# Optimization experiments

Hardware: AMD Instinct MI355X
Metric: run time of the kernel (lower is better)

## Reference

```python
import jax, jax.numpy as jnp
import numpy as np

N = 50000   # nodes
E = 800000  # edges (before self-loops)
D = 128     # feature dim
B = 1024    # query batch
EPS = 1e-5


def setup_inputs() -> dict:
    key = jax.random.key(0)
    ks = jax.random.split(key, 24)
    rn = lambda k, s, sc=0.05: jax.random.normal(k, s, jnp.float32) * sc
    return {
        "x": jax.random.randint(ks[0], (B, 3), 0, N),
        "edge_index": jax.random.randint(ks[1], (2, E), 0, N),
        "emb": rn(ks[2], (N, D), 1.0),
        # GAT layer 1
        "W1": rn(ks[3], (D, D)), "att_src1": rn(ks[4], (D,)), "att_dst1": rn(ks[5], (D,)), "b1": jnp.zeros((D,), jnp.float32),
        "gn1_w": jnp.ones((D,), jnp.float32), "gn1_b": jnp.zeros((D,), jnp.float32), "gn1_ms": jnp.ones((D,), jnp.float32),
        # GAT layer 2
        "W2": rn(ks[6], (D, D)), "att_src2": rn(ks[7], (D,)), "att_dst2": rn(ks[8], (D,)), "b2": jnp.zeros((D,), jnp.float32),
        "gn2_w": jnp.ones((D,), jnp.float32), "gn2_b": jnp.zeros((D,), jnp.float32), "gn2_ms": jnp.ones((D,), jnp.float32),
        # head
        "lin1_W": rn(ks[9], (3 * D, 3 * D)), "lin1_b": jnp.zeros((3 * D,), jnp.float32),
        "bn_w": jnp.ones((3 * D,), jnp.float32), "bn_b": jnp.zeros((3 * D,), jnp.float32),
        "lin2_W": rn(ks[10], (N, 3 * D)), "lin2_b": jnp.zeros((N,), jnp.float32),
    }


def _gat(h_in, src, dst, W, a_src, a_dst, b, n):
    # PyG GATConv, heads=1, negative_slope=0.2, self-loops already in src/dst,
    # dropout inactive (eval). Messages flow src -> dst.
    h = h_in @ W.T                                   # [N, D]
    as_n = h @ a_src                                 # [N]
    ad_n = h @ a_dst                                 # [N]
    e = jax.nn.leaky_relu(as_n[src] + ad_n[dst], 0.2)  # [E']
    m = jax.ops.segment_max(e, dst, num_segments=n)
    ex = jnp.exp(e - m[dst])
    den = jax.ops.segment_sum(ex, dst, num_segments=n)
    alpha = ex / den[dst]                            # segment softmax over dst
    out = jax.ops.segment_sum(h[src] * alpha[:, None], dst, num_segments=n)
    return out + b


def _graph_norm(h, w, b, ms):
    # PyG GraphNorm, single graph: per-feature mean/var over all nodes
    mu = h.mean(axis=0)
    out = h - mu * ms
    var = (out * out).mean(axis=0)
    return out / jnp.sqrt(var + EPS) * w + b


def reference(x, edge_index, emb, W1, att_src1, att_dst1, b1, gn1_w, gn1_b, gn1_ms,
              W2, att_src2, att_dst2, b2, gn2_w, gn2_b, gn2_ms,
              lin1_W, lin1_b, bn_w, bn_b, lin2_W, lin2_b):
    loop = jnp.arange(N)
    src = jnp.concatenate([edge_index[0], loop])
    dst = jnp.concatenate([edge_index[1], loop])

    h = jax.nn.relu(_graph_norm(_gat(emb, src, dst, W1, att_src1, att_dst1, b1, N), gn1_w, gn1_b, gn1_ms))
    h = jax.nn.relu(_graph_norm(_gat(h, src, dst, W2, att_src2, att_dst2, b2, N), gn2_w, gn2_b, gn2_ms))

    z = jnp.concatenate([h[x[:, 0]], h[x[:, 1]], h[x[:, 2]]], axis=1)  # [B, 3D]
    z = z @ lin1_W.T + lin1_b
    mu = z.mean(axis=0)
    var = ((z - mu) ** 2).mean(axis=0)  # BatchNorm1d training-mode batch stats
    z = jax.nn.relu((z - mu) / jnp.sqrt(var + EPS) * bn_w + bn_b)
    z = z @ lin2_W.T + lin2_b
    return jax.nn.log_softmax(z, axis=-1)
```

## Files before the change

### kernel.cpp

```cpp
#include <hip/hip_runtime.h>
#include <cstdint>
#include <cstddef>

#define NN 50000
#define EE 800000
#define EP 850000
#define DD 128
#define BB 1024
#define D3 384
#define NEG_SLOPE 0.2f

typedef __attribute__((ext_vector_type(8))) short short8;
typedef __attribute__((ext_vector_type(4))) float f32x4;

__device__ __forceinline__ unsigned short f2bf(float f) {
  unsigned int u = __float_as_uint(f);
  u += 0x7fffu + ((u >> 16) & 1u);
  return (unsigned short)(u >> 16);
}

__global__ void k_count(const int* __restrict__ eidx, int* __restrict__ cnt) {
  int e = blockIdx.x * 256 + threadIdx.x;
  if (e >= EP) return;
  int d = (e < EE) ? eidx[EE + e] : (e - EE);
  atomicAdd(&cnt[d], 1);
}

__global__ void k_scan1(const int* __restrict__ cnt, int* __restrict__ offs, int* __restrict__ bsum) {
  __shared__ int sd[1024];
  int tid = threadIdx.x;
  int i = blockIdx.x * 1024 + tid;
  int v = (i < NN) ? cnt[i] : 0;
  sd[tid] = v;
  __syncthreads();
  for (int off = 1; off < 1024; off <<= 1) {
    int t = (tid >= off) ? sd[tid - off] : 0;
    __syncthreads();
    sd[tid] += t;
    __syncthreads();
  }
  if (i < NN) offs[i] = sd[tid] - v;
  if (tid == 1023) bsum[blockIdx.x] = sd[1023];
}

__global__ void k_scan2(const int* __restrict__ bsum, int* __restrict__ bso) {
  int lane = threadIdx.x;
  int v = (lane < 49) ? bsum[lane] : 0;
  int s = v;
  #pragma unroll
  for (int off = 1; off < 64; off <<= 1) {
    int t = __shfl_up(s, off, 64);
    if (lane >= off) s += t;
  }
  if (lane < 49) bso[lane] = s - v;
}

__global__ void k_scan3(int* __restrict__ offs, const int* __restrict__ bso, int* __restrict__ cur) {
  int i = blockIdx.x * 256 + threadIdx.x;
  if (i >= NN) return;
  int o = offs[i] + bso[i >> 10];
  offs[i] = o;
  cur[i] = o;
}

__global__ void k_scatter(const int* __restrict__ eidx, int* __restrict__ cur, int* __restrict__ ssrc) {
  int e = blockIdx.x * 256 + threadIdx.x;
  if (e >= EP) return;
  int s, d;
  if (e < EE) { s = eidx[e]; d = eidx[EE + e]; } else { s = e - EE; d = s; }
  int p = atomicAdd(&cur[d], 1);
  ssrc[p] = s;
}

template<bool ABF16>
__global__ __launch_bounds__(256) void gemm_mfma(const void* __restrict__ Ap_, const float* __restrict__ Bm,
                                                 const float* __restrict__ bias, float* __restrict__ C,
                                                 int M, int Ncols, int K) {
  int tid = threadIdx.x;
  int wv = tid >> 6, lane = tid & 63;
  int l15 = lane & 15, q = lane >> 4;
  int n0 = blockIdx.x * 64;
  int mbase = blockIdx.y * 256 + wv * 64;
  int arow[4], brow[4];
  float bs[4];
  #pragma unroll
  for (int mi = 0; mi < 4; mi++) {
    int r = mbase + mi * 16 + l15;
    arow[mi] = (r < M) ? r : (M - 1);
  }
  #pragma unroll
  for (int nt = 0; nt < 4; nt++) {
    int col = n0 + nt * 16 + l15;
    brow[nt] = (col < Ncols) ? col : (Ncols - 1);
    bs[nt] = (bias != nullptr && col < Ncols) ? bias[col] : 0.0f;
  }
  f32x4 acc[4][4] = {};
  int nks = K >> 5;
  for (int ks = 0; ks < nks; ks++) {
    int k0 = ks * 32 + q * 8;
    short8 a[4], b[4];
    #pragma unroll
    for (int mi = 0; mi < 4; mi++) {
      if constexpr (ABF16) {
        a[mi] = *(const short8*)((const unsigned short*)Ap_ + (size_t)arow[mi] * K + k0);
      } else {
        const float* p = (const float*)Ap_ + (size_t)arow[mi] * K + k0;
        float4 v0 = *(const float4*)p, v1 = *(const float4*)(p + 4);
        short8 t;
        t[0] = f2bf(v0.x); t[1] = f2bf(v0.y); t[2] = f2bf(v0.z); t[3] = f2bf(v0.w);
        t[4] = f2bf(v1.x); t[5] = f2bf(v1.y); t[6] = f2bf(v1.z); t[7] = f2bf(v1.w);
        a[mi] = t;
      }
    }
    #pragma unroll
    for (int nt = 0; nt < 4; nt++) {
      const float* p = Bm + (size_t)brow[nt] * K + k0;
      float4 v0 = *(const float4*)p, v1 = *(const float4*)(p + 4);
      short8 t;
      t[0] = f2bf(v0.x); t[1] = f2bf(v0.y); t[2] = f2bf(v0.z); t[3] = f2bf(v0.w);
      t[4] = f2bf(v1.x); t[5] = f2bf(v1.y); t[6] = f2bf(v1.z); t[7] = f2bf(v1.w);
      b[nt] = t;
    }
    #pragma unroll
    for (int mi = 0; mi < 4; mi++)
      #pragma unroll
      for (int nt = 0; nt < 4; nt++)
        acc[mi][nt] = __builtin_amdgcn_mfma_f32_16x16x32_bf16(a[mi], b[nt], acc[mi][nt], 0, 0, 0);
  }
  #pragma unroll
  for (int mi = 0; mi < 4; mi++) {
    #pragma unroll
    for (int nt = 0; nt < 4; nt++) {
      int col = n0 + nt * 16 + l15;
      if (col < Ncols) {
        int rowb = mbase + mi * 16 + q * 4;
        #pragma unroll
        for (int r = 0; r < 4; r++) {
          int row = rowb + r;
          if (row < M) C[(size_t)row * Ncols + col] = acc[mi][nt][r] + bs[nt];
        }
      }
    }
  }
}

__global__ __launch_bounds__(256) void gemm_abt(const float* __restrict__ A, const float* __restrict__ Bm,
                                                const float* __restrict__ bias, float* __restrict__ C,
                                                int M, int Ncols, int K) {
  __shared__ float As[32][66];
  __shared__ float Bs[32][66];
  int tid = threadIdx.x;
  int tx = tid & 15, ty = tid >> 4;
  int m0 = blockIdx.x * 64, n0 = blockIdx.y * 64;
  float acc[4][4] = {};
  int lr = tid >> 2, lc = (tid & 3) * 8;
  for (int k0 = 0; k0 < K; k0 += 32) {
    float4 av0 = make_float4(0.f,0.f,0.f,0.f), av1 = av0, bv0 = av0, bv1 = av0;
    if (m0 + lr < M) {
      const float* Ap = A + (size_t)(m0 + lr) * K + k0 + lc;
      av0 = *(const float4*)Ap; av1 = *(const float4*)(Ap + 4);
    }
    if (n0 + lr < Ncols) {
      const float* Bp = Bm + (size_t)(n0 + lr) * K + k0 + lc;
      bv0 = *(const float4*)Bp; bv1 = *(const float4*)(Bp + 4);
    }
    __syncthreads();
    As[lc + 0][lr] = av0.x; As[lc + 1][lr] = av0.y; As[lc + 2][lr] = av0.z; As[lc + 3][lr] = av0.w;
    As[lc + 4][lr] = av1.x; As[lc + 5][lr] = av1.y; As[lc + 6][lr] = av1.z; As[lc + 7][lr] = av1.w;
    Bs[lc + 0][lr] = bv0.x; Bs[lc + 1][lr] = bv0.y; Bs[lc + 2][lr] = bv0.z; Bs[lc + 3][lr] = bv0.w;
    Bs[lc + 4][lr] = bv1.x; Bs[lc + 5][lr] = bv1.y; Bs[lc + 6][lr] = bv1.z; Bs[lc + 7][lr] = bv1.w;
    __syncthreads();
    #pragma unroll
    for (int kk = 0; kk < 32; kk++) {
      float a[4], b[4];
      #pragma unroll
      for (int i = 0; i < 4; i++) a[i] = As[kk][ty * 4 + i];
      #pragma unroll
      for (int j = 0; j < 4; j++) b[j] = Bs[kk][tx * 4 + j];
      #pragma unroll
      for (int i = 0; i < 4; i++)
        #pragma unroll
        for (int j = 0; j < 4; j++)
          acc[i][j] += a[i] * b[j];
    }
  }
  #pragma unroll
  for (int i = 0; i < 4; i++) {
    int row = m0 + ty * 4 + i;
    if (row < M) {
      #pragma unroll
      for (int j = 0; j < 4; j++) {
        int col = n0 + tx * 4 + j;
        if (col < Ncols) {
          float v = acc[i][j];
          if (bias) v += bias[col];
          C[(size_t)row * Ncols + col] = v;
        }
      }
    }
  }
}

__global__ void k_attn(const float* __restrict__ h, const float* __restrict__ asrc, const float* __restrict__ adst,
                       float* __restrict__ as_, float* __restrict__ ad_) {
  int wid = (blockIdx.x * 256 + threadIdx.x) >> 6;
  int lane = threadIdx.x & 63;
  if (wid >= NN) return;
  float v0 = h[(size_t)wid * DD + lane];
  float v1 = h[(size_t)wid * DD + 64 + lane];
  float s = v0 * asrc[lane] + v1 * asrc[64 + lane];
  float d = v0 * adst[lane] + v1 * adst[64 + lane];
  #pragma unroll
  for (int o = 32; o; o >>= 1) { s += __shfl_xor(s, o, 64); d += __shfl_xor(d, o, 64); }
  if (lane == 0) { as_[wid] = s; ad_[wid] = d; }
}

__global__ void k_agg(const float* __restrict__ h, const float* __restrict__ as_, const float* __restrict__ ad_,
                      const int* __restrict__ offs, const int* __restrict__ cnt, const int* __restrict__ ssrc,
                      const float* __restrict__ bias, float* __restrict__ outp) {
  int wid = (blockIdx.x * 256 + threadIdx.x) >> 6;
  int lane = threadIdx.x & 63;
  if (wid >= NN) return;
  int start = offs[wid], deg = cnt[wid];
  float add = ad_[wid];
  float m = -3.0e38f;
  for (int i = lane; i < deg; i += 64) {
    int s = ssrc[start + i];
    float e = as_[s] + add;
    e = (e >= 0.0f) ? e : NEG_SLOPE * e;
    m = fmaxf(m, e);
  }
  #pragma unroll
  for (int o = 32; o; o >>= 1) m = fmaxf(m, __shfl_xor(m, o, 64));
  float den = 0.0f;
  for (int i = lane; i < deg; i += 64) {
    int s = ssrc[start + i];
    float e = as_[s] + add;
    e = (e >= 0.0f) ? e : NEG_SLOPE * e;
    den += __expf(e - m);
  }
  #pragma unroll
  for (int o = 32; o; o >>= 1) den += __shfl_xor(den, o, 64);
  float a0 = 0.0f, a1 = 0.0f;
  for (int i = 0; i < deg; i++) {
    int s = ssrc[start + i];
    float e = as_[s] + add;
    e = (e >= 0.0f) ? e : NEG_SLOPE * e;
    float wg = __expf(e - m);
    a0 += wg * h[(size_t)s * DD + lane];
    a1 += wg * h[(size_t)s * DD + 64 + lane];
  }
  float inv = 1.0f / den;
  outp[(size_t)wid * DD + lane]      = a0 * inv + bias[lane];
  outp[(size_t)wid * DD + 64 + lane] = a1 * inv + bias[64 + lane];
}

__global__ void k_gn_stats(const float* __restrict__ h, float* __restrict__ acc) {
  __shared__ float r1[256], r2[256];
  int tid = threadIdx.x;
  int f = tid & 127, rg = tid >> 7;
  float a = 0.0f, b = 0.0f;
  for (int r = blockIdx.x * 2 + rg; r < NN; r += gridDim.x * 2) {
    float v = h[(size_t)r * DD + f];
    a += v; b += v * v;
  }
  r1[tid] = a; r2[tid] = b;
  __syncthreads();
  if (tid < 128) {
    atomicAdd(&acc[f], r1[tid] + r1[tid + 128]);
    atomicAdd(&acc[DD + f], r2[tid] + r2[tid + 128]);
  }
}

__global__ void k_gn_apply(float* __restrict__ h, const float* __restrict__ acc,
                           const float* __restrict__ ms, const float* __restrict__ w, const float* __restrict__ b) {
  const float invN = 1.0f / NN;
  for (size_t i = (size_t)blockIdx.x * 256 + threadIdx.x; i < (size_t)NN * DD; i += (size_t)gridDim.x * 256) {
    int f = (int)(i & 127);
    float mu = acc[f] * invN;
    float qm = acc[DD + f] * invN;
    float sub = mu * ms[f];
    float var = qm - 2.0f * sub * mu + sub * sub;
    float v = (h[i] - sub) * rsqrtf(var + 1e-5f) * w[f] + b[f];
    h[i] = fmaxf(v, 0.0f);
  }
}

__global__ void k_gather(const float* __restrict__ h, const int* __restrict__ x, float* __restrict__ z1) {
  int i = blockIdx.x * 256 + threadIdx.x;
  if (i >= BB * D3) return;
  int b = i / D3, t = i - b * D3;
  int part = t >> 7, f = t & 127;
  int node = x[b * 3 + part];
  z1[i] = h[(size_t)node * DD + f];
}

__global__ void k_bn(const float* __restrict__ z, const float* __restrict__ w, const float* __restrict__ b,
                     unsigned short* __restrict__ zb) {
  int c = blockIdx.x;
  int lane = threadIdx.x;
  float s = 0.0f, s2 = 0.0f;
  for (int r = lane; r < BB; r += 64) {
    float v = z[(size_t)r * D3 + c];
    s += v; s2 += v * v;
  }
  #pragma unroll
  for (int o = 32; o; o >>= 1) { s += __shfl_xor(s, o, 64); s2 += __shfl_xor(s2, o, 64); }
  float mu = s * (1.0f / BB);
  float var = s2 * (1.0f / BB) - mu * mu;
  float sc = rsqrtf(var + 1e-5f) * w[c];
  float sb = b[c];
  for (int r = lane; r < BB; r += 64) {
    float v = (z[(size_t)r * D3 + c] - mu) * sc + sb;
    zb[(size_t)r * D3 + c] = f2bf(fmaxf(v, 0.0f));
  }
}

__global__ __launch_bounds__(256) void k_softmax(float* __restrict__ z) {
  __shared__ float sm[256], ss[256];
  int row = blockIdx.x, tid = threadIdx.x;
  float* zr = z + (size_t)row * NN;
  float m = -3.0e38f, s = 0.0f;
  for (int c = tid; c < NN; c += 256) {
    float v = zr[c];
    if (v > m) { s *= __expf(m - v); m = v; }
    s += __expf(v - m);
  }
  sm[tid] = m; ss[tid] = s;
  __syncthreads();
  for (int st = 128; st > 0; st >>= 1) {
    if (tid < st) {
      float m2 = sm[tid + st], s2 = ss[tid + st];
      float M = fmaxf(sm[tid], m2);
      ss[tid] = ss[tid] * __expf(sm[tid] - M) + s2 * __expf(m2 - M);
      sm[tid] = M;
    }
    __syncthreads();
  }
  float L = sm[0] + logf(ss[0]);
  for (int c = tid; c < NN; c += 256) zr[c] -= L;
}

extern "C" void kernel_launch(void* const* d_in, const int* in_sizes, int n_in,
                              void* d_out, int out_size, void* d_ws, size_t ws_size,
                              hipStream_t stream) {
  const int*   x     = (const int*)d_in[0];
  const int*   eidx  = (const int*)d_in[1];
  const float* emb   = (const float*)d_in[2];
  const float* W1    = (const float*)d_in[3];
  const float* as1   = (const float*)d_in[4];
  const float* ad1   = (const float*)d_in[5];
  const float* b1    = (const float*)d_in[6];
  const float* gn1w  = (const float*)d_in[7];
  const float* gn1b  = (const float*)d_in[8];
  const float* gn1ms = (const float*)d_in[9];
  const float* W2    = (const float*)d_in[10];
  const float* as2   = (const float*)d_in[11];
  const float* ad2   = (const float*)d_in[12];
  const float* b2    = (const float*)d_in[13];
  const float* gn2w  = (const float*)d_in[14];
  const float* gn2b  = (const float*)d_in[15];
  const float* gn2ms = (const float*)d_in[16];
  const float* l1W   = (const float*)d_in[17];
  const float* l1b   = (const float*)d_in[18];
  const float* bnw   = (const float*)d_in[19];
  const float* bnb   = (const float*)d_in[20];
  const float* l2W   = (const float*)d_in[21];
  const float* l2b   = (const float*)d_in[22];
  float* out = (float*)d_out;

  float* h1 = out;
  float* h2 = out + (size_t)NN * DD;

  char* wsb = (char*)d_ws;
  size_t o = 0;
  auto alloc = [&](size_t bytes) -> void* {
    void* p = wsb + o;
    o = (o + bytes + 255) & ~(size_t)255;
    return p;
  };
  int*   ssrc = (int*)alloc((size_t)EP * 4);
  int*   cnt  = (int*)alloc((size_t)NN * 4);
  int*   offs = (int*)alloc((size_t)NN * 4);
  int*   cur  = (int*)alloc((size_t)NN * 4);
  float* as_  = (float*)alloc((size_t)NN * 4);
  float* ad_  = (float*)alloc((size_t)NN * 4);
  int*   bsum = (int*)alloc(64 * 4);
  int*   bso  = (int*)alloc(64 * 4);
  float* gnacc= (float*)alloc(2 * DD * 4);
  float* z1   = (float*)alloc((size_t)BB * D3 * 4);
  float* z2   = (float*)alloc((size_t)BB * D3 * 4);
  unsigned short* zbf = (unsigned short*)alloc((size_t)BB * D3 * 2);

  hipMemsetAsync(cnt, 0, (size_t)NN * 4, stream);
  k_count  <<<(EP + 255) / 256, 256, 0, stream>>>(eidx, cnt);
  k_scan1  <<<49, 1024, 0, stream>>>(cnt, offs, bsum);
  k_scan2  <<<1, 64, 0, stream>>>(bsum, bso);
  k_scan3  <<<(NN + 255) / 256, 256, 0, stream>>>(offs, bso, cur);
  k_scatter<<<(EP + 255) / 256, 256, 0, stream>>>(eidx, cur, ssrc);

  gemm_mfma<false><<<dim3(2, 196), 256, 0, stream>>>(emb, W1, nullptr, h1, NN, DD, DD);
  k_attn  <<<(NN + 3) / 4, 256, 0, stream>>>(h1, as1, ad1, as_, ad_);
  k_agg   <<<(NN + 3) / 4, 256, 0, stream>>>(h1, as_, ad_, offs, cnt, ssrc, b1, h2);
  hipMemsetAsync(gnacc, 0, 2 * DD * 4, stream);
  k_gn_stats<<<256, 256, 0, stream>>>(h2, gnacc);
  k_gn_apply<<<8192, 256, 0, stream>>>(h2, gnacc, gn1ms, gn1w, gn1b);

  gemm_mfma<false><<<dim3(2, 196), 256, 0, stream>>>(h2, W2, nullptr, h1, NN, DD, DD);
  k_attn  <<<(NN + 3) / 4, 256, 0, stream>>>(h1, as2, ad2, as_, ad_);
  k_agg   <<<(NN + 3) / 4, 256, 0, stream>>>(h1, as_, ad_, offs, cnt, ssrc, b2, h2);
  hipMemsetAsync(gnacc, 0, 2 * DD * 4, stream);
  k_gn_stats<<<256, 256, 0, stream>>>(h2, gnacc);
  k_gn_apply<<<8192, 256, 0, stream>>>(h2, gnacc, gn2ms, gn2w, gn2b);

  k_gather<<<(BB * D3 + 255) / 256, 256, 0, stream>>>(h2, x, z1);
  gemm_abt<<<dim3(16, 6), 256, 0, stream>>>(z1, l1W, l1b, z2, BB, D3, D3);
  k_bn    <<<D3, 64, 0, stream>>>(z2, bnw, bnb, zbf);
  gemm_mfma<true><<<dim3(782, 4), 256, 0, stream>>>(zbf, l2W, l2b, out, BB, NN, D3);
  k_softmax<<<BB, 256, 0, stream>>>(out);
}
```

Baseline: 1.203 ms.

## Switch GNN pipeline to bf16 intermediates with LDS-tiled MFMA GEMM

Replaces the register-direct MFMA GEMM and the scalar FP32 head GEMM with one LDS-tiled 128x128 bf16 MFMA kernel that uses global_load_lds and swizzled shared memory. Embeddings and weights are pre-converted to bf16, and the GAT projected features are stored in bf16, which halves the gather traffic in the attention and aggregation kernels. The aggregation loop is also unrolled by four to overlap gathers. The aim is to cut memory bandwidth in the edge aggregation and the large final GEMM, at the cost of lower precision for intermediate features and extra conversion passes.

```diff
diff --git a/kernel.cpp b/kernel.cpp
--- a/kernel.cpp
+++ b/kernel.cpp
@@ -12,11 +12,30 @@
 
 typedef __attribute__((ext_vector_type(8))) short short8;
 typedef __attribute__((ext_vector_type(4))) float f32x4;
-
-__device__ __forceinline__ unsigned short f2bf(float f) {
-  unsigned int u = __float_as_uint(f);
+typedef unsigned short u16;
+typedef unsigned int u32;
+
+__device__ __forceinline__ u16 f2bf(float f) {
+  u32 u = __float_as_uint(f);
   u += 0x7fffu + ((u >> 16) & 1u);
-  return (unsigned short)(u >> 16);
+  return (u16)(u >> 16);
+}
+__device__ __forceinline__ float bflo(u32 u) { return __uint_as_float(u << 16); }
+__device__ __forceinline__ float bfhi(u32 u) { return __uint_as_float(u & 0xffff0000u); }
+
+__device__ __forceinline__ void gl2lds16(const u16* g, u16* lds_base_uniform) {
+  __builtin_amdgcn_global_load_lds((const __attribute__((address_space(1))) u32*)g,
+                                   (__attribute__((address_space(3))) u32*)lds_base_uniform,
+                                   16, 0, 0);
+}
+
+__global__ void k_f2bf(const float* __restrict__ s, u16* __restrict__ d, int n4) {
+  int i = blockIdx.x * 256 + threadIdx.x;
+  if (i >= n4) return;
+  float4 v = ((const float4*)s)[i];
+  ushort4 o;
+  o.x = f2bf(v.x); o.y = f2bf(v.y); o.z = f2bf(v.z); o.w = f2bf(v.w);
+  ((ushort4*)d)[i] = o;
 }
 
 __global__ void k_count(const int* __restrict__ eidx, int* __restrict__ cnt) {
@@ -72,150 +91,126 @@
   ssrc[p] = s;
 }
 
-template<bool ABF16>
-__global__ __launch_bounds__(256) void gemm_mfma(const void* __restrict__ Ap_, const float* __restrict__ Bm,
-                                                 const float* __restrict__ bias, float* __restrict__ C,
-                                                 int M, int Ncols, int K) {
+template<bool B_IS_F32, bool OUT_BF16>
+__global__ __launch_bounds__(256) void gemm_tile(const u16* __restrict__ A, const void* __restrict__ Bv,
+                                                 const float* __restrict__ bias, void* __restrict__ Cv,
+                                                 int M, int N, int K) {
+  __shared__ u16 As[16 * 512];
+  __shared__ u16 Bs[16 * 512];
   int tid = threadIdx.x;
-  int wv = tid >> 6, lane = tid & 63;
+  int w = tid >> 6, lane = tid & 63;
   int l15 = lane & 15, q = lane >> 4;
-  int n0 = blockIdx.x * 64;
-  int mbase = blockIdx.y * 256 + wv * 64;
-  int arow[4], brow[4];
-  float bs[4];
-  #pragma unroll
-  for (int mi = 0; mi < 4; mi++) {
-    int r = mbase + mi * 16 + l15;
-    arow[mi] = (r < M) ? r : (M - 1);
-  }
-  #pragma unroll
-  for (int nt = 0; nt < 4; nt++) {
-    int col = n0 + nt * 16 + l15;
-    brow[nt] = (col < Ncols) ? col : (Ncols - 1);
-    bs[nt] = (bias != nullptr && col < Ncols) ? bias[col] : 0.0f;
-  }
+  int n0 = blockIdx.x * 128, m0 = blockIdx.y * 128;
+  int mh = w & 1, nh = w >> 1;
+
+  int lr = lane >> 3;
+  int cg = (lane & 7) ^ lr;
+
   f32x4 acc[4][4] = {};
-  int nks = K >> 5;
-  for (int ks = 0; ks < nks; ks++) {
-    int k0 = ks * 32 + q * 8;
-    short8 a[4], b[4];
+
+  for (int kt = 0; kt < K; kt += 64) {
     #pragma unroll
-    for (int mi = 0; mi < 4; mi++) {
-      if constexpr (ABF16) {
-        a[mi] = *(const short8*)((const unsigned short*)Ap_ + (size_t)arow[mi] * K + k0);
-      } else {
-        const float* p = (const float*)Ap_ + (size_t)arow[mi] * K + k0;
-        float4 v0 = *(const float4*)p, v1 = *(const float4*)(p + 4);
+    for (int i = 0; i < 4; i++) {
+      int inst = (w << 2) | i;
+      int row = inst * 8 + lr;
+      int grow = m0 + row; if (grow > M - 1) grow = M - 1;
+      gl2lds16(A + (size_t)grow * K + kt + cg * 8, &As[inst * 512]);
+    }
+    if constexpr (!B_IS_F32) {
+      const u16* Bb = (const u16*)Bv;
+      #pragma unroll
+      for (int i = 0; i < 4; i++) {
+        int inst = (w << 2) | i;
+        int row = inst * 8 + lr;
+        int gn = n0 + row; if (gn > N - 1) gn = N - 1;
+        gl2lds16(Bb + (size_t)gn * K + kt + cg * 8, &Bs[inst * 512]);
+      }
+    } else {
+      const float* Bf = (const float*)Bv;
+      int row = tid >> 1, half = tid & 1;
+      int gn = n0 + row; if (gn > N - 1) gn = N - 1;
+      const float* gp = Bf + (size_t)gn * K + kt;
+      #pragma unroll
+      for (int j = 0; j < 4; j++) {
+        int c = half * 4 + j;
+        float4 v0 = *(const float4*)(gp + c * 8);
+        float4 v1 = *(const float4*)(gp + c * 8 + 4);
         short8 t;
         t[0] = f2bf(v0.x); t[1] = f2bf(v0.y); t[2] = f2bf(v0.z); t[3] = f2bf(v0.w);
         t[4] = f2bf(v1.x); t[5] = f2bf(v1.y); t[6] = f2bf(v1.z); t[7] = f2bf(v1.w);
-        a[mi] = t;
+        int c2 = c ^ (row & 7);
+        *(short8*)(&Bs[row * 64 + c2 * 8]) = t;
       }
     }
+    __builtin_amdgcn_s_waitcnt(0x0f70);
+    __syncthreads();
+
+    #pragma unroll
+    for (int kk = 0; kk < 2; kk++) {
+      short8 a[4], b[4];
+      int cbase = kk * 4 + q;
+      int csw = cbase ^ (l15 & 7);
+      #pragma unroll
+      for (int mi = 0; mi < 4; mi++) {
+        int row = (mh * 4 + mi) * 16 + l15;
+        a[mi] = *(const short8*)(&As[row * 64 + csw * 8]);
+      }
+      #pragma unroll
+      for (int nt = 0; nt < 4; nt++) {
+        int row = (nh * 4 + nt) * 16 + l15;
+        b[nt] = *(const short8*)(&Bs[row * 64 + csw * 8]);
+      }
+      #pragma unroll
+      for (int mi = 0; mi < 4; mi++)
+        #pragma unroll
+        for (int nt = 0; nt < 4; nt++)
+          acc[mi][nt] = __builtin_amdgcn_mfma_f32_16x16x32_bf16(a[mi], b[nt], acc[mi][nt], 0, 0, 0);
+    }
+    __syncthreads();
+  }
+
+  float bsv[4];
+  #pragma unroll
+  for (int nt = 0; nt < 4; nt++) {
+    int col = n0 + nh * 64 + nt * 16 + l15;
+    bsv[nt] = (bias != nullptr && col < N) ? bias[col] : 0.0f;
+  }
+  #pragma unroll
+  for (int mi = 0; mi < 4; mi++) {
+    int rowg = m0 + mh * 64 + mi * 16 + q * 4;
     #pragma unroll
     for (int nt = 0; nt < 4; nt++) {
-      const float* p = Bm + (size_t)brow[nt] * K + k0;
-      float4 v0 = *(const float4*)p, v1 = *(const float4*)(p + 4);
-      short8 t;
-      t[0] = f2bf(v0.x); t[1] = f2bf(v0.y); t[2] = f2bf(v0.z); t[3] = f2bf(v0.w);
-      t[4] = f2bf(v1.x); t[5] = f2bf(v1.y); t[6] = f2bf(v1.z); t[7] = f2bf(v1.w);
-      b[nt] = t;
-    }
-    #pragma unroll
-    for (int mi = 0; mi < 4; mi++)
-      #pragma unroll
-      for (int nt = 0; nt < 4; nt++)
-        acc[mi][nt] = __builtin_amdgcn_mfma_f32_16x16x32_bf16(a[mi], b[nt], acc[mi][nt], 0, 0, 0);
-  }
-  #pragma unroll
-  for (int mi = 0; mi < 4; mi++) {
-    #pragma unroll
-    for (int nt = 0; nt < 4; nt++) {
-      int col = n0 + nt * 16 + l15;
-      if (col < Ncols) {
-        int rowb = mbase + mi * 16 + q * 4;
+      int col = n0 + nh * 64 + nt * 16 + l15;
+      if (col < N) {
         #pragma unroll
         for (int r = 0; r < 4; r++) {
-          int row = rowb + r;
-          if (row < M) C[(size_t)row * Ncols + col] = acc[mi][nt][r] + bs[nt];
+          int rw = rowg + r;
+          if (rw < M) {
+            float v = acc[mi][nt][r] + bsv[nt];
+            if constexpr (OUT_BF16) ((u16*)Cv)[(size_t)rw * N + col] = f2bf(v);
+            else                    ((float*)Cv)[(size_t)rw * N + col] = v;
+          }
         }
       }
     }
   }
 }
 
-__global__ __launch_bounds__(256) void gemm_abt(const float* __restrict__ A, const float* __restrict__ Bm,
-                                                const float* __restrict__ bias, float* __restrict__ C,
-                                                int M, int Ncols, int K) {
-  __shared__ float As[32][66];
-  __shared__ float Bs[32][66];
-  int tid = threadIdx.x;
-  int tx = tid & 15, ty = tid >> 4;
-  int m0 = blockIdx.x * 64, n0 = blockIdx.y * 64;
-  float acc[4][4] = {};
-  int lr = tid >> 2, lc = (tid & 3) * 8;
-  for (int k0 = 0; k0 < K; k0 += 32) {
-    float4 av0 = make_float4(0.f,0.f,0.f,0.f), av1 = av0, bv0 = av0, bv1 = av0;
-    if (m0 + lr < M) {
-      const float* Ap = A + (size_t)(m0 + lr) * K + k0 + lc;
-      av0 = *(const float4*)Ap; av1 = *(const float4*)(Ap + 4);
-    }
-    if (n0 + lr < Ncols) {
-      const float* Bp = Bm + (size_t)(n0 + lr) * K + k0 + lc;
-      bv0 = *(const float4*)Bp; bv1 = *(const float4*)(Bp + 4);
-    }
-    __syncthreads();
-    As[lc + 0][lr] = av0.x; As[lc + 1][lr] = av0.y; As[lc + 2][lr] = av0.z; As[lc + 3][lr] = av0.w;
-    As[lc + 4][lr] = av1.x; As[lc + 5][lr] = av1.y; As[lc + 6][lr] = av1.z; As[lc + 7][lr] = av1.w;
-    Bs[lc + 0][lr] = bv0.x; Bs[lc + 1][lr] = bv0.y; Bs[lc + 2][lr] = bv0.z; Bs[lc + 3][lr] = bv0.w;
-    Bs[lc + 4][lr] = bv1.x; Bs[lc + 5][lr] = bv1.y; Bs[lc + 6][lr] = bv1.z; Bs[lc + 7][lr] = bv1.w;
-    __syncthreads();
-    #pragma unroll
-    for (int kk = 0; kk < 32; kk++) {
-      float a[4], b[4];
-      #pragma unroll
-      for (int i = 0; i < 4; i++) a[i] = As[kk][ty * 4 + i];
-      #pragma unroll
-      for (int j = 0; j < 4; j++) b[j] = Bs[kk][tx * 4 + j];
-      #pragma unroll
-      for (int i = 0; i < 4; i++)
-        #pragma unroll
-        for (int j = 0; j < 4; j++)
-          acc[i][j] += a[i] * b[j];
-    }
-  }
-  #pragma unroll
-  for (int i = 0; i < 4; i++) {
-    int row = m0 + ty * 4 + i;
-    if (row < M) {
-      #pragma unroll
-      for (int j = 0; j < 4; j++) {
-        int col = n0 + tx * 4 + j;
-        if (col < Ncols) {
-          float v = acc[i][j];
-          if (bias) v += bias[col];
-          C[(size_t)row * Ncols + col] = v;
-        }
-      }
-    }
-  }
-}
-
-__global__ void k_attn(const float* __restrict__ h, const float* __restrict__ asrc, const float* __restrict__ adst,
+__global__ void k_attn(const u16* __restrict__ hb, const float* __restrict__ asrc, const float* __restrict__ adst,
                        float* __restrict__ as_, float* __restrict__ ad_) {
   int wid = (blockIdx.x * 256 + threadIdx.x) >> 6;
   int lane = threadIdx.x & 63;
   if (wid >= NN) return;
-  float v0 = h[(size_t)wid * DD + lane];
-  float v1 = h[(size_t)wid * DD + 64 + lane];
-  float s = v0 * asrc[lane] + v1 * asrc[64 + lane];
-  float d = v0 * adst[lane] + v1 * adst[64 + lane];
+  u32 u = ((const u32*)(hb + (size_t)wid * DD))[lane];
+  float v0 = bflo(u), v1 = bfhi(u);
+  float s = v0 * asrc[2 * lane] + v1 * asrc[2 * lane + 1];
+  float d = v0 * adst[2 * lane] + v1 * adst[2 * lane + 1];
   #pragma unroll
   for (int o = 32; o; o >>= 1) { s += __shfl_xor(s, o, 64); d += __shfl_xor(d, o, 64); }
   if (lane == 0) { as_[wid] = s; ad_[wid] = d; }
 }
 
-__global__ void k_agg(const float* __restrict__ h, const float* __restrict__ as_, const float* __restrict__ ad_,
+__global__ void k_agg(const u16* __restrict__ hb, const float* __restrict__ as_, const float* __restrict__ ad_,
                       const int* __restrict__ offs, const int* __restrict__ cnt, const int* __restrict__ ssrc,
                       const float* __restrict__ bias, float* __restrict__ outp) {
   int wid = (blockIdx.x * 256 + threadIdx.x) >> 6;
@@ -241,18 +236,40 @@
   }
   #pragma unroll
   for (int o = 32; o; o >>= 1) den += __shfl_xor(den, o, 64);
+
+  const u32* hp = (const u32*)hb;
   float a0 = 0.0f, a1 = 0.0f;
-  for (int i = 0; i < deg; i++) {
+  int i = 0;
+  for (; i + 4 <= deg; i += 4) {
+    int s0 = ssrc[start + i + 0], s1 = ssrc[start + i + 1];
+    int s2 = ssrc[start + i + 2], s3 = ssrc[start + i + 3];
+    u32 u0 = hp[(size_t)s0 * 64 + lane];
+    u32 u1 = hp[(size_t)s1 * 64 + lane];
+    u32 u2 = hp[(size_t)s2 * 64 + lane];
+    u32 u3 = hp[(size_t)s3 * 64 + lane];
+    float e0 = as_[s0] + add, e1 = as_[s1] + add, e2 = as_[s2] + add, e3 = as_[s3] + add;
+    e0 = (e0 >= 0.0f) ? e0 : NEG_SLOPE * e0;
+    e1 = (e1 >= 0.0f) ? e1 : NEG_SLOPE * e1;
+    e2 = (e2 >= 0.0f) ? e2 : NEG_SLOPE * e2;
+    e3 = (e3 >= 0.0f) ? e3 : NEG_SLOPE * e3;
+    float w0 = __expf(e0 - m), w1 = __expf(e1 - m), w2 = __expf(e2 - m), w3 = __expf(e3 - m);
+    a0 += w0 * bflo(u0) + w1 * bflo(u1) + w2 * bflo(u2) + w3 * bflo(u3);
+    a1 += w0 * bfhi(u0) + w1 * bfhi(u1) + w2 * bfhi(u2) + w3 * bfhi(u3);
+  }
+  for (; i < deg; i++) {
     int s = ssrc[start + i];
+    u32 u = hp[(size_t)s * 64 + lane];
     float e = as_[s] + add;
     e = (e >= 0.0f) ? e : NEG_SLOPE * e;
     float wg = __expf(e - m);
-    a0 += wg * h[(size_t)s * DD + lane];
-    a1 += wg * h[(size_t)s * DD + 64 + lane];
+    a0 += wg * bflo(u);
+    a1 += wg * bfhi(u);
   }
   float inv = 1.0f / den;
-  outp[(size_t)wid * DD + lane]      = a0 * inv + bias[lane];
-  outp[(size_t)wid * DD + 64 + lane] = a1 * inv + bias[64 + lane];
+  float2 st;
+  st.x = a0 * inv + bias[2 * lane];
+  st.y = a1 * inv + bias[2 * lane + 1];
+  *(float2*)(outp + (size_t)wid * DD + 2 * lane) = st;
 }
 
 __global__ void k_gn_stats(const float* __restrict__ h, float* __restrict__ acc) {
@@ -273,7 +290,8 @@
 }
 
 __global__ void k_gn_apply(float* __restrict__ h, const float* __restrict__ acc,
-                           const float* __restrict__ ms, const float* __restrict__ w, const float* __restrict__ b) {
+                           const float* __restrict__ ms, const float* __restrict__ w, const float* __restrict__ b,
+                           u16* __restrict__ hb) {
   const float invN = 1.0f / NN;
   for (size_t i = (size_t)blockIdx.x * 256 + threadIdx.x; i < (size_t)NN * DD; i += (size_t)gridDim.x * 256) {
     int f = (int)(i & 127);
@@ -282,21 +300,23 @@
     float sub = mu * ms[f];
     float var = qm - 2.0f * sub * mu + sub * sub;
     float v = (h[i] - sub) * rsqrtf(var + 1e-5f) * w[f] + b[f];
-    h[i] = fmaxf(v, 0.0f);
-  }
-}
-
-__global__ void k_gather(const float* __restrict__ h, const int* __restrict__ x, float* __restrict__ z1) {
+    v = fmaxf(v, 0.0f);
+    h[i] = v;
+    if (hb) hb[i] = f2bf(v);
+  }
+}
+
+__global__ void k_gather(const float* __restrict__ h, const int* __restrict__ x, u16* __restrict__ z1b) {
   int i = blockIdx.x * 256 + threadIdx.x;
   if (i >= BB * D3) return;
   int b = i / D3, t = i - b * D3;
   int part = t >> 7, f = t & 127;
   int node = x[b * 3 + part];
-  z1[i] = h[(size_t)node * DD + f];
+  z1b[i] = f2bf(h[(size_t)node * DD + f]);
 }
 
 __global__ void k_bn(const float* __restrict__ z, const float* __restrict__ w, const float* __restrict__ b,
-                     unsigned short* __restrict__ zb) {
+                     u16* __restrict__ zb) {
   int c = blockIdx.x;
   int lane = threadIdx.x;
   float s = 0.0f, s2 = 0.0f;
@@ -368,9 +388,12 @@
   const float* l2W   = (const float*)d_in[21];
   const float* l2b   = (const float*)d_in[22];
   float* out = (float*)d_out;
-
-  float* h1 = out;
-  float* h2 = out + (size_t)NN * DD;
+  char*  dob = (char*)d_out;
+
+  u16*   embb = (u16*)(dob);
+  u16*   h1b  = (u16*)(dob + (16u << 20));
+  float* h2   = (float*)(dob + (32u << 20));
+  u16*   h2b  = (u16*)(dob + (64u << 20));
 
   char* wsb = (char*)d_ws;
   size_t o = 0;
@@ -388,9 +411,17 @@
   int*   bsum = (int*)alloc(64 * 4);
   int*   bso  = (int*)alloc(64 * 4);
   float* gnacc= (float*)alloc(2 * DD * 4);
-  float* z1   = (float*)alloc((size_t)BB * D3 * 4);
+  u16*   W1b  = (u16*)alloc((size_t)DD * DD * 2);
+  u16*   W2b  = (u16*)alloc((size_t)DD * DD * 2);
+  u16*   l1Wb = (u16*)alloc((size_t)D3 * D3 * 2);
+  u16*   z1b  = (u16*)alloc((size_t)BB * D3 * 2);
   float* z2   = (float*)alloc((size_t)BB * D3 * 4);
-  unsigned short* zbf = (unsigned short*)alloc((size_t)BB * D3 * 2);
+  u16*   zbf  = (u16*)alloc((size_t)BB * D3 * 2);
+
+  k_f2bf<<<(NN * DD / 4 + 255) / 256, 256, 0, stream>>>(emb, embb, NN * DD / 4);
+  k_f2bf<<<(DD * DD / 4 + 255) / 256, 256, 0, stream>>>(W1, W1b, DD * DD / 4);
+  k_f2bf<<<(DD * DD / 4 + 255) / 256, 256, 0, stream>>>(W2, W2b, DD * DD / 4);
+  k_f2bf<<<(D3 * D3 / 4 + 255) / 256, 256, 0, stream>>>(l1W, l1Wb, D3 * D3 / 4);
 
   hipMemsetAsync(cnt, 0, (size_t)NN * 4, stream);
   k_count  <<<(EP + 255) / 256, 256, 0, stream>>>(eidx, cnt);
@@ -399,23 +430,23 @@
   k_scan3  <<<(NN + 255) / 256, 256, 0, stream>>>(offs, bso, cur);
   k_scatter<<<(EP + 255) / 256, 256, 0, stream>>>(eidx, cur, ssrc);
 
-  gemm_mfma<false><<<dim3(2, 196), 256, 0, stream>>>(emb, W1, nullptr, h1, NN, DD, DD);
-  k_attn  <<<(NN + 3) / 4, 256, 0, stream>>>(h1, as1, ad1, as_, ad_);
-  k_agg   <<<(NN + 3) / 4, 256, 0, stream>>>(h1, as_, ad_, offs, cnt, ssrc, b1, h2);
+  gemm_tile<false, true><<<dim3(1, 391), 256, 0, stream>>>(embb, W1b, nullptr, h1b, NN, DD, DD);
+  k_attn<<<(NN + 3) / 4, 256, 0, stream>>>(h1b, as1, ad1, as_, ad_);
+  k_agg <<<(NN + 3) / 4, 256, 0, stream>>>(h1b, as_, ad_, offs, cnt, ssrc, b1, h2);
   hipMemsetAsync(gnacc, 0, 2 * DD * 4, stream);
   k_gn_stats<<<256, 256, 0, stream>>>(h2, gnacc);
-  k_gn_apply<<<8192, 256, 0, stream>>>(h2, gnacc, gn1ms, gn1w, gn1b);
-
-  gemm_mfma<false><<<dim3(2, 196), 256, 0, stream>>>(h2, W2, nullptr, h1, NN, DD, DD);
-  k_attn  <<<(NN + 3) / 4, 256, 0, stream>>>(h1, as2, ad2, as_, ad_);
-  k_agg   <<<(NN + 3) / 4, 256, 0, stream>>>(h1, as_, ad_, offs, cnt, ssrc, b2, h2);
+  k_gn_apply<<<8192, 256, 0, stream>>>(h2, gnacc, gn1ms, gn1w, gn1b, h2b);
+
+  gemm_tile<false, true><<<dim3(1, 391), 256, 0, stream>>>(h2b, W2b, nullptr, h1b, NN, DD, DD);
+  k_attn<<<(NN + 3) / 4, 256, 0, stream>>>(h1b, as2, ad2, as_, ad_);
+  k_agg <<<(NN + 3) / 4, 256, 0, stream>>>(h1b, as_, ad_, offs, cnt, ssrc, b2, h2);
   hipMemsetAsync(gnacc, 0, 2 * DD * 4, stream);
   k_gn_stats<<<256, 256, 0, stream>>>(h2, gnacc);
-  k_gn_apply<<<8192, 256, 0, stream>>>(h2, gnacc, gn2ms, gn2w, gn2b);
-
-  k_gather<<<(BB * D3 + 255) / 256, 256, 0, stream>>>(h2, x, z1);
-  gemm_abt<<<dim3(16, 6), 256, 0, stream>>>(z1, l1W, l1b, z2, BB, D3, D3);
-  k_bn    <<<D3, 64, 0, stream>>>(z2, bnw, bnb, zbf);
-  gemm_mfma<true><<<dim3(782, 4), 256, 0, stream>>>(zbf, l2W, l2b, out, BB, NN, D3);
+  k_gn_apply<<<8192, 256, 0, stream>>>(h2, gnacc, gn2ms, gn2w, gn2b, nullptr);
+
+  k_gather<<<(BB * D3 + 255) / 256, 256, 0, stream>>>(h2, x, z1b);
+  gemm_tile<false, false><<<dim3(3, 8), 256, 0, stream>>>(z1b, l1Wb, l1b, z2, BB, D3, D3);
+  k_bn<<<D3, 64, 0, stream>>>(z2, bnw, bnb, zbf);
+  gemm_tile<true, false><<<dim3(391, 8), 256, 0, stream>>>(zbf, l2W, l2b, out, BB, NN, D3);
   k_softmax<<<BB, 256, 0, stream>>>(out);
 }
```

Measured after the change: 1.014 ms. 15.7% less time.
